# Performance work log

Hardware: AMD Instinct MI355X
Metric: run time of the kernel (lower is better)

The kernel has to match this reference:

```python
import jax, jax.numpy as jnp
import numpy as np

B, S, D, H, O = 128, 512, 128, 1024, 64
IN = 2 * D + 1  # input_size*2 + 1


def _xavier(key, shape):
    fan_out, fan_in = shape
    std = np.sqrt(2.0 / (fan_in + fan_out)).astype(np.float32)
    return jax.random.normal(key, shape, jnp.float32) * std


def setup_inputs() -> dict:
    key = jax.random.key(0)
    ks = jax.random.split(key, 6)
    x = jax.random.normal(ks[0], (B, S, D), jnp.float32)
    mask = jax.random.uniform(ks[1], (B, S, D), jnp.float32)
    ti = jax.random.uniform(ks[2], (B, S, 1), jnp.float32)
    W_ih = _xavier(ks[3], (4 * H, IN))   # LSTMCell weight_ih
    W_hh = _xavier(ks[4], (4 * H, H))    # LSTMCell weight_hh
    b_ih = jnp.zeros((4 * H,), jnp.float32)
    b_hh = jnp.zeros((4 * H,), jnp.float32)
    W_fc = _xavier(ks[5], (O, H))
    b_fc = jnp.zeros((O,), jnp.float32)
    return {"x": x, "mask": mask, "ti": ti, "W_ih": W_ih, "W_hh": W_hh,
            "b_ih": b_ih, "b_hh": b_hh, "W_fc": W_fc, "b_fc": b_fc}


def reference(x, mask, ti, W_ih, W_hh, b_ih, b_hh, W_fc, b_fc):
    b, s, _ = x.shape
    h = W_hh.shape[1]
    xt = jnp.concatenate([x, mask, ti], axis=-1)          # [B,S,IN]
    # Precompute input contribution to gates for all timesteps (one big GEMM)
    xg = jnp.einsum('bsi,gi->sbg', xt, W_ih) + b_ih + b_hh  # [S,B,4H]

    def step(carry, xg_t):
        h_t, c_t = carry
        g = xg_t + h_t @ W_hh.T                             # [B,4H]
        i, f, gg, o = jnp.split(g, 4, axis=-1)              # torch gate order i,f,g,o
        i = jax.nn.sigmoid(i)
        f = jax.nn.sigmoid(f)
        gg = jnp.tanh(gg)
        o = jax.nn.sigmoid(o)
        c_new = f * c_t + i * gg
        h_new = o * jnp.tanh(c_new)
        return (h_new, c_new), None

    h0 = jnp.zeros((b, h), x.dtype)
    c0 = jnp.zeros((b, h), x.dtype)
    (h_last, _), _ = jax.lax.scan(step, (h0, c0), xg)
    return h_last @ W_fc.T + b_fc                           # [B,O]
```

## Files before the change

kernel.cpp:

```cpp
#include <hip/hip_runtime.h>
#include <hip/hip_bf16.h>

typedef __bf16 bf16x8 __attribute__((ext_vector_type(8)));
typedef float f32x4 __attribute__((ext_vector_type(4)));
typedef unsigned int u32x4 __attribute__((ext_vector_type(4)));

#define BB   128
#define SS   512
#define DD   128
#define HH   1024
#define OO   64
#define IIN  257

#define NGROUP 8
#define GBLK   64
#define MG     16
#define KK_H   32
#define KK_X   9

#define XTP_TP    (KK_X*512)
#define HBUF_SLAB (KK_H*512)
#define WIH_BLK   (4*KK_X*512)

#define WS_HBUF  8192
#define WS_HLAST 532480
#define WS_XTP   1056768
#define WS_WIHP  38805504

__device__ __forceinline__ u32x4 ldg_dev16(const void* p) {
  u32x4 r;
  asm volatile("global_load_dwordx4 %0, %1, off sc1" : "=v"(r) : "v"(p));
  return r;
}
__device__ __forceinline__ void stg_dev4(void* p, unsigned int v) {
  asm volatile("global_store_dword %0, %1, off sc1" :: "v"(p), "v"(v));
}
__device__ __forceinline__ bf16x8 asbf(u32x4 v) {
  union { u32x4 u; bf16x8 h; } c; c.u = v; return c.h;
}

#define CLAIMW4(CNTSTR, A, O)                                        \
  asm volatile("s_waitcnt vmcnt(" CNTSTR ")"                         \
    : "+v"((A)[(O)]), "+v"((A)[(O)+1]), "+v"((A)[(O)+2]), "+v"((A)[(O)+3]))

__global__ void flag_init(unsigned int* __restrict__ flags) {
  stg_dev4(flags + blockIdx.x * 256 + threadIdx.x, 0u);
}

__global__ void prepack_kernel(const float* __restrict__ x, const float* __restrict__ mask,
                               const float* __restrict__ ti, __bf16* __restrict__ xtp) {
  int idx = blockIdx.x * 256 + threadIdx.x;
  int j = idx & 7, l = (idx >> 3) & 63;
  int rest = idx >> 9;
  int kk = rest % 9;
  int rest2 = rest / 9;
  int p = rest2 & 7;
  int t = rest2 >> 3;
  int b = p * MG + (l & 15);
  int k = kk * 32 + ((l >> 4) << 3) + j;
  float v;
  if (k < 128)       v = x[(b * SS + t) * DD + k];
  else if (k < 256)  v = mask[(b * SS + t) * DD + (k - 128)];
  else if (k == 256) v = ti[b * SS + t];
  else               v = 0.f;
  xtp[idx] = (__bf16)v;
}

__global__ void wih_prepack(const float* __restrict__ W_ih, __bf16* __restrict__ wihp) {
  int idx = blockIdx.x * 256 + threadIdx.x;
  int j = idx & 7, l = (idx >> 3) & 63;
  int rest = idx >> 9;
  int kk = rest % 9;
  int rest2 = rest / 9;
  int nt = rest2 & 3, q = rest2 >> 2;
  int col = nt * HH + q * 16 + (l & 15);
  int k = kk * 32 + ((l >> 4) << 3) + j;
  wihp[idx] = (k < IIN) ? (__bf16)W_ih[col * IIN + k] : (__bf16)0.f;
}

__device__ __forceinline__ float sigmoid_f(float v) { return 1.f / (1.f + __expf(-v)); }
__device__ __forceinline__ float tanh_f(float v)    { return 1.f - 2.f / (__expf(2.f * v) + 1.f); }

__launch_bounds__(256, 2)
__global__ void lstm_scan(const float* __restrict__ W_hh,
                          const float* __restrict__ b_ih, const float* __restrict__ b_hh,
                          const __bf16* __restrict__ xtp, const __bf16* __restrict__ wihp,
                          __bf16* __restrict__ hbuf,
                          float* __restrict__ hlast, unsigned int* __restrict__ flags) {
  __shared__ float red_lds[8192];

  const int tid = threadIdx.x;
  const int bid = blockIdx.x;
  const int p = bid & 7;
  const int q = bid >> 3;
  const int j0 = q * 16;

  const int w = tid >> 6, l = tid & 63;
  const int n16 = l & 15, qh = l >> 4;
  unsigned int* gflags = flags + p * 256;

  bf16x8 breg[4][8];
  #pragma unroll
  for (int ntI = 0; ntI < 4; ++ntI) {
    const float* wrow = W_hh + (size_t)(ntI * HH + j0 + n16) * HH;
    #pragma unroll
    for (int i = 0; i < 8; ++i) {
      const float* src = wrow + (w * 8 + i) * 32 + qh * 8;
      bf16x8 bv;
      #pragma unroll
      for (int jj = 0; jj < 8; ++jj) bv[jj] = (__bf16)src[jj];
      breg[ntI][i] = bv;
    }
  }

  const int grow = qh * 4 + w;
  float bias_r[4];
  #pragma unroll
  for (int g = 0; g < 4; ++g)
    bias_r[g] = b_ih[g * HH + j0 + n16] + b_hh[g * HH + j0 + n16];
  float creg = 0.f;

  const int xs = (w == 0) ? 0 : (2 * w + 1);
  const int xe = xs + ((w == 0) ? 3 : 2);

  for (int t = 0; t < SS; ++t) {
    const int rb = t & 1, wb = rb ^ 1;
    f32x4 acc[4];
    #pragma unroll
    for (int ntI = 0; ntI < 4; ++ntI) acc[ntI] = (f32x4){0.f, 0.f, 0.f, 0.f};

    for (int kk = xs; kk < xe; ++kk) {
      const __bf16* xb = xtp + ((size_t)(t * 8 + p) * KK_X + kk) * 512 + l * 8;
      bf16x8 a = *(const bf16x8*)xb;
      #pragma unroll
      for (int ntI = 0; ntI < 4; ++ntI) {
        bf16x8 b = *(const bf16x8*)(wihp + ((size_t)(q * 4 + ntI) * KK_X + kk) * 512 + l * 8);
        acc[ntI] = __builtin_amdgcn_mfma_f32_16x16x32_bf16(a, b, acc[ntI], 0, 0, 0);
      }
    }

    if (t > 0) {
      {
        const unsigned int tgt = (unsigned int)t;
        const unsigned int* fp = gflags + (w << 6) + l;
        for (;;) {
          unsigned int f;
          asm volatile("global_load_dword %0, %1, off sc1\n\t"
                       "s_waitcnt vmcnt(0)"
                       : "=v"(f) : "v"(fp));
          if (!__ballot((f - tgt) > 1u)) break;
          __builtin_amdgcn_s_sleep(1);
        }
        __builtin_amdgcn_sched_barrier(0);
      }

      const __bf16* hbL = hbuf + (p * 2 + rb) * HBUF_SLAB + (w * 8) * 512 + l * 8;
      u32x4 A[8];
      #pragma unroll
      for (int i = 0; i < 8; ++i) A[i] = ldg_dev16(hbL + i * 512);

      CLAIMW4("4", A, 0);
      #pragma unroll
      for (int i = 0; i < 4; ++i)
        #pragma unroll
        for (int ntI = 0; ntI < 4; ++ntI)
          acc[ntI] = __builtin_amdgcn_mfma_f32_16x16x32_bf16(asbf(A[i]), breg[ntI][i], acc[ntI], 0, 0, 0);
      CLAIMW4("0", A, 4);
      #pragma unroll
      for (int i = 4; i < 8; ++i)
        #pragma unroll
        for (int ntI = 0; ntI < 4; ++ntI)
          acc[ntI] = __builtin_amdgcn_mfma_f32_16x16x32_bf16(asbf(A[i]), breg[ntI][i], acc[ntI], 0, 0, 0);
    }

    __syncthreads();

    #pragma unroll
    for (int g = 0; g < 4; ++g)
      #pragma unroll
      for (int r = 0; r < 4; ++r)
        red_lds[(((w * 4 + g) * 4 + r) * 4 + qh) * 32 + n16 * 2 + (qh & 1)] = acc[g][r];
    __syncthreads();

    {
      __bf16* hw = hbuf + (p * 2 + wb) * HBUF_SLAB;
      float gv[4];
      #pragma unroll
      for (int g = 0; g < 4; ++g) {
        float own = (w == 0) ? acc[g][0] : (w == 1) ? acc[g][1]
                  : (w == 2) ? acc[g][2] : acc[g][3];
        float s = own + bias_r[g];
        #pragma unroll
        for (int wo = 0; wo < 4; ++wo)
          if (wo != w)
            s += red_lds[(((wo * 4 + g) * 4 + w) * 4 + qh) * 32 + n16 * 2 + (qh & 1)];
        gv[g] = s;
      }
      float i_ = sigmoid_f(gv[0]);
      float f_ = sigmoid_f(gv[1]);
      float g_ = tanh_f(gv[2]);
      float o_ = sigmoid_f(gv[3]);
      float c  = f_ * creg + i_ * g_;
      creg = c;
      float h  = o_ * tanh_f(c);

      union { __bf16 b; unsigned short u; } cv; cv.b = (__bf16)h;
      unsigned int hu = (unsigned int)cv.u;
      unsigned int partner = __shfl_xor(hu, 1);
      if ((n16 & 1) == 0) {
        unsigned int dw = hu | (partner << 16);
        int k = j0 + n16;
        int kk = k >> 5, q2 = (k >> 3) & 3, jj = k & 7;
        stg_dev4(hw + kk * 512 + (q2 * 16 + grow) * 8 + jj, dw);
      }
      if (t == SS - 1) hlast[(p * MG + grow) * HH + j0 + n16] = h;
    }

    asm volatile("s_waitcnt vmcnt(0)" ::: "memory");
    if (t < SS - 1 && l == 0) {
      stg_dev4(gflags + q * 4 + w, (unsigned int)(t + 1));
    }
  }
}

__global__ void fc_kernel(const float* __restrict__ hlast, const float* __restrict__ W_fc,
                          const float* __restrict__ b_fc, float* __restrict__ out) {
  int b = blockIdx.x;
  int t = threadIdx.x;
  int o = t >> 2, part = t & 3;
  const float* hr = hlast + b * HH;
  const float* wr = W_fc + o * HH;
  float s = 0.f;
  #pragma unroll 4
  for (int k0 = part * 4; k0 < HH; k0 += 16) {
    float4 hv = *(const float4*)(hr + k0);
    float4 wv = *(const float4*)(wr + k0);
    s += hv.x * wv.x + hv.y * wv.y + hv.z * wv.z + hv.w * wv.w;
  }
  s += __shfl_xor(s, 1);
  s += __shfl_xor(s, 2);
  if (part == 0) out[b * OO + o] = s + b_fc[o];
}

extern "C" void kernel_launch(void* const* d_in, const int* in_sizes, int n_in,
                              void* d_out, int out_size, void* d_ws, size_t ws_size,
                              hipStream_t stream) {
  const float* x    = (const float*)d_in[0];
  const float* mask = (const float*)d_in[1];
  const float* ti   = (const float*)d_in[2];
  const float* W_ih = (const float*)d_in[3];
  const float* W_hh = (const float*)d_in[4];
  const float* b_ih = (const float*)d_in[5];
  const float* b_hh = (const float*)d_in[6];
  const float* W_fc = (const float*)d_in[7];
  const float* b_fc = (const float*)d_in[8];
  float* out = (float*)d_out;

  char* ws = (char*)d_ws;
  unsigned int* flags = (unsigned int*)ws;
  __bf16* hbuf  = (__bf16*)(ws + WS_HBUF);
  float*  hlast = (float*)(ws + WS_HLAST);
  __bf16* xtp   = (__bf16*)(ws + WS_XTP);
  __bf16* wihp  = (__bf16*)(ws + WS_WIHP);

  flag_init<<<8, 256, 0, stream>>>(flags);

  prepack_kernel<<<(SS * NGROUP * XTP_TP) / 256, 256, 0, stream>>>(x, mask, ti, xtp);
  wih_prepack<<<(GBLK * WIH_BLK) / 256, 256, 0, stream>>>(W_ih, wihp);
  lstm_scan<<<NGROUP * GBLK, 256, 0, stream>>>(W_hh, b_ih, b_hh, xtp, wihp, hbuf, hlast, flags);
  fc_kernel<<<BB, 256, 0, stream>>>(hlast, W_fc, b_fc, out);
}
```

Measured before the change: 2.120 ms.

## Use XCC-local cache-scope sync when all group blocks share one XCD

```diff
diff --git a/kernel.cpp b/kernel.cpp
--- a/kernel.cpp
+++ b/kernel.cpp
@@ -27,13 +27,36 @@
 #define WS_XTP   1056768
 #define WS_WIHP  38805504
 
-__device__ __forceinline__ u32x4 ldg_dev16(const void* p) {
+__device__ __forceinline__ void stg_sc1(void* p, unsigned int v) {
+  asm volatile("global_store_dword %0, %1, off sc1" :: "v"(p), "v"(v));
+}
+__device__ __forceinline__ void stg_sc0(void* p, unsigned int v) {
+  asm volatile("global_store_dword %0, %1, off sc0" :: "v"(p), "v"(v));
+}
+__device__ __forceinline__ unsigned int poll_sc1(const unsigned int* p) {
+  unsigned int f;
+  asm volatile("global_load_dword %0, %1, off sc1\n\ts_waitcnt vmcnt(0)" : "=v"(f) : "v"(p));
+  return f;
+}
+__device__ __forceinline__ unsigned int poll_sc0(const unsigned int* p) {
+  unsigned int f;
+  asm volatile("global_load_dword %0, %1, off sc0\n\ts_waitcnt vmcnt(0)" : "=v"(f) : "v"(p));
+  return f;
+}
+template<bool FAST>
+__device__ __forceinline__ u32x4 ldh16(const void* p) {
   u32x4 r;
-  asm volatile("global_load_dwordx4 %0, %1, off sc1" : "=v"(r) : "v"(p));
+  if (FAST) asm volatile("global_load_dwordx4 %0, %1, off sc0" : "=v"(r) : "v"(p));
+  else      asm volatile("global_load_dwordx4 %0, %1, off sc1" : "=v"(r) : "v"(p));
   return r;
 }
-__device__ __forceinline__ void stg_dev4(void* p, unsigned int v) {
-  asm volatile("global_store_dword %0, %1, off sc1" :: "v"(p), "v"(v));
+template<bool FAST>
+__device__ __forceinline__ void sth4(void* p, unsigned int v) {
+  if (FAST) stg_sc0(p, v); else stg_sc1(p, v);
+}
+template<bool FAST>
+__device__ __forceinline__ unsigned int pollld(const unsigned int* p) {
+  return FAST ? poll_sc0(p) : poll_sc1(p);
 }
 __device__ __forceinline__ bf16x8 asbf(u32x4 v) {
   union { u32x4 u; bf16x8 h; } c; c.u = v; return c.h;
@@ -43,8 +66,10 @@
   asm volatile("s_waitcnt vmcnt(" CNTSTR ")"                         \
     : "+v"((A)[(O)]), "+v"((A)[(O)+1]), "+v"((A)[(O)+2]), "+v"((A)[(O)+3]))
 
-__global__ void flag_init(unsigned int* __restrict__ flags) {
-  stg_dev4(flags + blockIdx.x * 256 + threadIdx.x, 0u);
+__global__ void flag_init(unsigned int* __restrict__ flags, unsigned int* __restrict__ aux) {
+  int i = blockIdx.x * 256 + threadIdx.x;
+  if (i < 2048) stg_sc1(flags + i, 0u);
+  else          stg_sc1(aux + (i - 2048), 0u);
 }
 
 __global__ void prepack_kernel(const float* __restrict__ x, const float* __restrict__ mask,
@@ -81,45 +106,14 @@
 __device__ __forceinline__ float sigmoid_f(float v) { return 1.f / (1.f + __expf(-v)); }
 __device__ __forceinline__ float tanh_f(float v)    { return 1.f - 2.f / (__expf(2.f * v) + 1.f); }
 
-__launch_bounds__(256, 2)
-__global__ void lstm_scan(const float* __restrict__ W_hh,
-                          const float* __restrict__ b_ih, const float* __restrict__ b_hh,
-                          const __bf16* __restrict__ xtp, const __bf16* __restrict__ wihp,
-                          __bf16* __restrict__ hbuf,
-                          float* __restrict__ hlast, unsigned int* __restrict__ flags) {
-  __shared__ float red_lds[8192];
-
-  const int tid = threadIdx.x;
-  const int bid = blockIdx.x;
-  const int p = bid & 7;
-  const int q = bid >> 3;
-  const int j0 = q * 16;
-
-  const int w = tid >> 6, l = tid & 63;
-  const int n16 = l & 15, qh = l >> 4;
-  unsigned int* gflags = flags + p * 256;
-
-  bf16x8 breg[4][8];
-  #pragma unroll
-  for (int ntI = 0; ntI < 4; ++ntI) {
-    const float* wrow = W_hh + (size_t)(ntI * HH + j0 + n16) * HH;
-    #pragma unroll
-    for (int i = 0; i < 8; ++i) {
-      const float* src = wrow + (w * 8 + i) * 32 + qh * 8;
-      bf16x8 bv;
-      #pragma unroll
-      for (int jj = 0; jj < 8; ++jj) bv[jj] = (__bf16)src[jj];
-      breg[ntI][i] = bv;
-    }
-  }
-
-  const int grow = qh * 4 + w;
-  float bias_r[4];
-  #pragma unroll
-  for (int g = 0; g < 4; ++g)
-    bias_r[g] = b_ih[g * HH + j0 + n16] + b_hh[g * HH + j0 + n16];
+template<bool FAST>
+__device__ __forceinline__ void run_scan(
+    int p, int q, int j0, int w, int l, int n16, int qh, int grow,
+    unsigned int* gflags,
+    const bf16x8 (&breg)[4][8], const float (&bias_r)[4],
+    const __bf16* __restrict__ xtp, const __bf16* __restrict__ wihp,
+    __bf16* __restrict__ hbuf, float* __restrict__ hlast, float* red_lds) {
   float creg = 0.f;
-
   const int xs = (w == 0) ? 0 : (2 * w + 1);
   const int xe = xs + ((w == 0) ? 3 : 2);
 
@@ -144,10 +138,7 @@
         const unsigned int tgt = (unsigned int)t;
         const unsigned int* fp = gflags + (w << 6) + l;
         for (;;) {
-          unsigned int f;
-          asm volatile("global_load_dword %0, %1, off sc1\n\t"
-                       "s_waitcnt vmcnt(0)"
-                       : "=v"(f) : "v"(fp));
+          unsigned int f = pollld<FAST>(fp);
           if (!__ballot((f - tgt) > 1u)) break;
           __builtin_amdgcn_s_sleep(1);
         }
@@ -157,7 +148,7 @@
       const __bf16* hbL = hbuf + (p * 2 + rb) * HBUF_SLAB + (w * 8) * 512 + l * 8;
       u32x4 A[8];
       #pragma unroll
-      for (int i = 0; i < 8; ++i) A[i] = ldg_dev16(hbL + i * 512);
+      for (int i = 0; i < 8; ++i) A[i] = ldh16<FAST>(hbL + i * 512);
 
       CLAIMW4("4", A, 0);
       #pragma unroll
@@ -211,16 +202,109 @@
         unsigned int dw = hu | (partner << 16);
         int k = j0 + n16;
         int kk = k >> 5, q2 = (k >> 3) & 3, jj = k & 7;
-        stg_dev4(hw + kk * 512 + (q2 * 16 + grow) * 8 + jj, dw);
+        sth4<FAST>(hw + kk * 512 + (q2 * 16 + grow) * 8 + jj, dw);
       }
       if (t == SS - 1) hlast[(p * MG + grow) * HH + j0 + n16] = h;
     }
 
     asm volatile("s_waitcnt vmcnt(0)" ::: "memory");
     if (t < SS - 1 && l == 0) {
-      stg_dev4(gflags + q * 4 + w, (unsigned int)(t + 1));
-    }
-  }
+      sth4<FAST>(gflags + q * 4 + w, (unsigned int)(t + 1));
+    }
+  }
+}
+
+__launch_bounds__(256, 2)
+__global__ void lstm_scan(const float* __restrict__ W_hh,
+                          const float* __restrict__ b_ih, const float* __restrict__ b_hh,
+                          const __bf16* __restrict__ xtp, const __bf16* __restrict__ wihp,
+                          __bf16* __restrict__ hbuf, float* __restrict__ hlast,
+                          unsigned int* __restrict__ flags, unsigned int* __restrict__ aux) {
+  __shared__ float red_lds[8192];
+
+  const int tid = threadIdx.x;
+  const int bid = blockIdx.x;
+  const int p = bid & 7;
+  const int q = bid >> 3;
+  const int j0 = q * 16;
+
+  const int w = tid >> 6, l = tid & 63;
+  const int n16 = l & 15, qh = l >> 4;
+  unsigned int* gflags  = flags + p * 256;
+  unsigned int* idpub   = aux + p * 64;
+  unsigned int* marker  = aux + 512 + p * 64;
+  unsigned int* outc    = aux + 1024 + p * 64;
+
+  unsigned int xcc;
+  asm("s_getreg_b32 %0, hwreg(HW_REG_XCC_ID)" : "=s"(xcc));
+  const unsigned int idb = (xcc & 0xFu) + 1u;
+  if (tid == 0) stg_sc1(idpub + q, idb);
+
+  bf16x8 breg[4][8];
+  #pragma unroll
+  for (int ntI = 0; ntI < 4; ++ntI) {
+    const float* wrow = W_hh + (size_t)(ntI * HH + j0 + n16) * HH;
+    #pragma unroll
+    for (int i = 0; i < 8; ++i) {
+      const float* src = wrow + (w * 8 + i) * 32 + qh * 8;
+      bf16x8 bv;
+      #pragma unroll
+      for (int jj = 0; jj < 8; ++jj) bv[jj] = (__bf16)src[jj];
+      breg[ntI][i] = bv;
+    }
+  }
+
+  const int grow = qh * 4 + w;
+  float bias_r[4];
+  #pragma unroll
+  for (int g = 0; g < 4; ++g)
+    bias_r[g] = b_ih[g * HH + j0 + n16] + b_hh[g * HH + j0 + n16];
+
+  int same;
+  {
+    const unsigned int* ip = idpub + l;
+    unsigned int f;
+    for (;;) {
+      f = poll_sc1(ip);
+      if (!__ballot(f == 0u)) break;
+      __builtin_amdgcn_s_sleep(1);
+    }
+    unsigned int cm = __builtin_amdgcn_readfirstlane(f);
+    same = (__ballot(f != cm) == 0ull) && (cm == idb);
+  }
+
+  int blockok = 0;
+  if (same) {
+    if (tid == 0) stg_sc0(marker + q, 0xA5u);
+    const unsigned int* mp = marker + l;
+    int seen = 0;
+    for (int it = 0; it < 4096 && !seen; ++it) {
+      unsigned int f = poll_sc0(mp);
+      seen = (__ballot(f != 0xA5u) == 0ull);
+      if (!seen) __builtin_amdgcn_s_sleep(1);
+    }
+    blockok = seen;
+  }
+
+  if (tid == 0) stg_sc1(outc + q, blockok ? 1u : 2u);
+  int fastm;
+  {
+    const unsigned int* op = outc + l;
+    unsigned int f;
+    for (;;) {
+      f = poll_sc1(op);
+      if (!__ballot(f == 0u)) break;
+      __builtin_amdgcn_s_sleep(1);
+    }
+    fastm = (__ballot(f != 1u) == 0ull);
+  }
+
+  if (fastm)
+    run_scan<true >(p, q, j0, w, l, n16, qh, grow, gflags,
+                    breg, bias_r, xtp, wihp, hbuf, hlast, red_lds);
+  else
+    run_scan<false>(p, q, j0, w, l, n16, qh, grow, gflags,
+                    breg, bias_r, xtp, wihp, hbuf, hlast, red_lds);
 }
 
 __global__ void fc_kernel(const float* __restrict__ hlast, const float* __restrict__ W_fc,
@@ -260,13 +344,14 @@
   unsigned int* flags = (unsigned int*)ws;
   __bf16* hbuf  = (__bf16*)(ws + WS_HBUF);
   float*  hlast = (float*)(ws + WS_HLAST);
+  unsigned int* aux = (unsigned int*)(ws + WS_HLAST);
   __bf16* xtp   = (__bf16*)(ws + WS_XTP);
   __bf16* wihp  = (__bf16*)(ws + WS_WIHP);
 
-  flag_init<<<8, 256, 0, stream>>>(flags);
+  flag_init<<<16, 256, 0, stream>>>(flags, aux);
 
   prepack_kernel<<<(SS * NGROUP * XTP_TP) / 256, 256, 0, stream>>>(x, mask, ti, xtp);
   wih_prepack<<<(GBLK * WIH_BLK) / 256, 256, 0, stream>>>(W_ih, wihp);
-  lstm_scan<<<NGROUP * GBLK, 256, 0, stream>>>(W_hh, b_ih, b_hh, xtp, wihp, hbuf, hlast, flags);
+  lstm_scan<<<NGROUP * GBLK, 256, 0, stream>>>(W_hh, b_ih, b_hh, xtp, wihp, hbuf, hlast, flags, aux);
   fc_kernel<<<BB, 256, 0, stream>>>(hlast, W_fc, b_fc, out);
 }
```

New measurement: 2.593 ms. 1.22x slower.
